# Kernel tuning notes

Hardware: AMD Instinct MI355X
Metric: run time of the kernel (lower is better)

Reference implementation:

```python
import jax, jax.numpy as jnp
import numpy as np

N_T = 8
N_R = 2
NOISE = 1e-12  # 10**(-120/10)
B = 65536


def setup_inputs() -> dict:
    key = jax.random.key(0)
    ks = jax.random.split(key, 7)
    return {
        "theta1": jax.random.normal(ks[0], (B, 264), dtype=jnp.float32),
        "G1r": jax.random.normal(ks[1], (B, N_R, 100), dtype=jnp.float32),
        "G1i": jax.random.normal(ks[2], (B, N_R, 100), dtype=jnp.float32),
        "G2r": jax.random.normal(ks[3], (B, N_R, 100), dtype=jnp.float32),
        "G2i": jax.random.normal(ks[4], (B, N_R, 100), dtype=jnp.float32),
        "Ur": jax.random.normal(ks[5], (B, 100, N_T), dtype=jnp.float32),
        "Ui": jax.random.normal(ks[6], (B, 100, N_T), dtype=jnp.float32),
    }


def _rate(phi, Fsig, Fintf):
    # phi: [B, N_r, N_t], Fsig/Fintf: [B, N_t, N_r]
    A = jnp.einsum("bnt,btr->bnr", phi, Fsig)    # signal term  [B, N_r, N_r]
    C = jnp.einsum("bnt,btr->bnr", phi, Fintf)   # interference [B, N_r, N_r]
    # Mu = C C^H + noise (elementwise scalar add, faithful to torch source)
    Mu = jnp.einsum("bnr,bmr->bnm", C, jnp.conj(C)) + NOISE
    inner = jnp.einsum("brn,bnm,bms->brs", jnp.conj(A).transpose(0, 2, 1) if False else jnp.conj(jnp.swapaxes(A, 1, 2)), jnp.linalg.inv(Mu), A)
    # note: torch does 1 + matrix (elementwise), not identity add
    return jnp.real(jnp.log(jnp.linalg.det(1.0 + inner)))  # [B]


def reference(theta1, G1r, G1i, G2r, G2i, Ur, Ui):
    M1N1 = N_T * N_R  # 16
    F1 = theta1[:, 200:200 + M1N1] + 1j * theta1[:, 200 + M1N1:200 + 2 * M1N1]
    F2 = theta1[:, 200 + 2 * M1N1:200 + 3 * M1N1] + 1j * theta1[:, 200 + 3 * M1N1:]
    # power normalization: F * sqrt(2 / (F^H F))
    F1 = F1 * jnp.sqrt(2.0 / jnp.sum(jnp.conj(F1) * F1, axis=1, keepdims=True))
    F2 = F2 * jnp.sqrt(2.0 / jnp.sum(jnp.conj(F2) * F2, axis=1, keepdims=True))
    F1m = F1.reshape(-1, N_T, N_R)
    F2m = F2.reshape(-1, N_T, N_R)

    theta = theta1[:, 0:100] + 1j * theta1[:, 100:200]  # [B, 100]
    G1 = G1r + 1j * G1i
    G2 = G2r + 1j * G2i
    U = Ur + 1j * Ui

    # phi = G @ diag(theta) @ U, vectorized over batch
    phi1 = jnp.einsum("bnk,bk,bkt->bnt", G1, theta, U)  # [B, N_r, N_t]
    phi2 = jnp.einsum("bnk,bk,bkt->bnt", G2, theta, U)

    R1 = _rate(phi1, F1m, F2m)
    R2 = _rate(phi2, F2m, F1m)
    R = jnp.maximum(-R1, -R2)
    return jnp.sum(R) / theta1.shape[0]
```

## Files before the change

### kernel.cpp

```cpp
#include <hip/hip_runtime.h>
#include <math.h>

#define NOISE 1e-12f
#define WSZ 1064
#define WSZ4 266

typedef float f32x2 __attribute__((ext_vector_type(2)));

__device__ __forceinline__ f32x2 mk2(float x, float y){ f32x2 r; r.x = x; r.y = y; return r; }

__device__ __forceinline__ f32x2 cmul_pk(f32x2 a, f32x2 b) {
    f32x2 w;
    asm("v_pk_mul_f32 %0, %1, %2 op_sel:[0,0] op_sel_hi:[0,1]\n\t"
        "v_pk_fma_f32 %0, %1, %2, %0 op_sel:[1,1,0] op_sel_hi:[1,0,1] neg_lo:[0,1,0]"
        : "=&v"(w) : "v"(a), "v"(b));
    return w;
}
__device__ __forceinline__ void cfma_pk(f32x2& p, f32x2 a, f32x2 w) {
    asm("v_pk_fma_f32 %0, %1, %2, %0 op_sel:[0,0,0] op_sel_hi:[0,1,1]\n\t"
        "v_pk_fma_f32 %0, %1, %2, %0 op_sel:[1,1,0] op_sel_hi:[1,0,1] neg_lo:[0,1,0]"
        : "+v"(p) : "v"(a), "v"(w));
}

__device__ __forceinline__ float2 cmul(float2 a, float2 b) {
    return make_float2(a.x*b.x - a.y*b.y, a.x*b.y + a.y*b.x);
}
__device__ __forceinline__ float2 cconjmul(float2 a, float2 b) {
    return make_float2(a.x*b.x + a.y*b.y, a.x*b.y - a.y*b.x);
}
__device__ __forceinline__ float2 cmulconj(float2 a, float2 b) {
    return make_float2(a.x*b.x + a.y*b.y, a.y*b.x - a.x*b.y);
}
__device__ __forceinline__ float2 cadd(float2 a, float2 b){ return make_float2(a.x+b.x, a.y+b.y); }
__device__ __forceinline__ float2 csub(float2 a, float2 b){ return make_float2(a.x-b.x, a.y-b.y); }
__device__ __forceinline__ float2 cscale(float s, float2 a){ return make_float2(s*a.x, s*a.y); }

typedef const void __attribute__((address_space(1)))* gas_t;
typedef void __attribute__((address_space(3)))* las_t;
__device__ __forceinline__ void gll4(const float* g, float* l) {
    __builtin_amdgcn_global_load_lds((gas_t)g, (las_t)l, 4, 0, 0);
}

__global__ __launch_bounds__(256) void rate_kernel(
    const float* __restrict__ t1,
    const float* __restrict__ G1r, const float* __restrict__ G1i,
    const float* __restrict__ G2r, const float* __restrict__ G2i,
    const float* __restrict__ Ur,  const float* __restrict__ Ui,
    float* __restrict__ partial)
{
    __shared__ float4 lds4[4 * WSZ4];
    __shared__ float2 ent[4][4][16];
    __shared__ float wsum[4];
    const int wave = threadIdx.x >> 6;
    const int lane = threadIdx.x & 63;
    const int t  = lane & 7;
    const int k0 = lane >> 3;
    const int e8 = k0;
    const int nn = (e8 >> 1) & 1;
    const int rr = e8 & 1;
    float* W = (float*)(lds4 + wave * WSZ4);
    const float4* F4 = (const float4*)W;

    const int half  = lane & 1;
    const int qh    = lane >> 1;

    #define STAGE(dst, bb) {                                                   \
        const float* tb_ = t1 + (long)(bb) * 264;                              \
        const float* ts  = tb_ + (half ? 100 : 0) + qh;                        \
        gll4(ts,       (dst));        gll4(ts + 32,  (dst) + 64);              \
        gll4(ts + 64,  (dst) + 128);                                           \
        if (lane < 8) gll4(ts + 96, (dst) + 192);                              \
        gll4(tb_ + 200 + lane, (dst) + 200);                                   \
        const float* g1 = (half ? G1i : G1r) + (long)(bb) * 200 + qh;          \
        const float* g2 = (half ? G2i : G2r) + (long)(bb) * 200 + qh;          \
        gll4(g1,        (dst)+264);   gll4(g1+32,  (dst)+328);                 \
        gll4(g1+64,     (dst)+392);   gll4(g1+96,  (dst)+456);                 \
        gll4(g1+128,    (dst)+520);   gll4(g1+160, (dst)+584);                 \
        if (lane < 16) gll4(g1+192, (dst)+648);                                \
        gll4(g2,        (dst)+664);   gll4(g2+32,  (dst)+728);                 \
        gll4(g2+64,     (dst)+792);   gll4(g2+96,  (dst)+856);                 \
        gll4(g2+128,    (dst)+920);   gll4(g2+160, (dst)+984);                 \
        if (lane < 16) gll4(g2+192, (dst)+1048);                               \
    }

    const long bbase = (long)blockIdx.x * 16 + (long)wave * 4;
    STAGE(W, bbase);

    const float* urb = Ur + bbase * 800;
    const float* uib = Ui + bbase * 800;
    const int uoff = 32 * k0 + t;
    #define LDU2(idx) mk2(urb[(idx)], uib[(idx)])

    f32x2 u0 = LDU2(uoff), u1 = LDU2(uoff+8), u2 = LDU2(uoff+16), u3 = LDU2(uoff+24);

    #define JGROUP_PK(f0, U0, U1, U2, U3) {                                   \
        float4 t01 = F4[(f0)],      t23 = F4[(f0)+1];                         \
        float4 a01 = F4[66+(f0)],   a23 = F4[67+(f0)];                        \
        float4 c01 = F4[116+(f0)],  c23 = F4[117+(f0)];                       \
        float4 d01 = F4[166+(f0)],  d23 = F4[167+(f0)];                       \
        float4 e01 = F4[216+(f0)],  e23 = F4[217+(f0)];                       \
        { f32x2 Wk = cmul_pk(mk2(t01.x,t01.y), U0);                           \
          cfma_pk(p10, mk2(a01.x,a01.y), Wk); cfma_pk(p11, mk2(c01.x,c01.y), Wk); \
          cfma_pk(p20, mk2(d01.x,d01.y), Wk); cfma_pk(p21, mk2(e01.x,e01.y), Wk); } \
        { f32x2 Wk = cmul_pk(mk2(t01.z,t01.w), U1);                           \
          cfma_pk(p10, mk2(a01.z,a01.w), Wk); cfma_pk(p11, mk2(c01.z,c01.w), Wk); \
          cfma_pk(p20, mk2(d01.z,d01.w), Wk); cfma_pk(p21, mk2(e01.z,e01.w), Wk); } \
        { f32x2 Wk = cmul_pk(mk2(t23.x,t23.y), U2);                           \
          cfma_pk(p10, mk2(a23.x,a23.y), Wk); cfma_pk(p11, mk2(c23.x,c23.y), Wk); \
          cfma_pk(p20, mk2(d23.x,d23.y), Wk); cfma_pk(p21, mk2(e23.x,e23.y), Wk); } \
        { f32x2 Wk = cmul_pk(mk2(t23.z,t23.w), U3);                           \
          cfma_pk(p10, mk2(a23.z,a23.w), Wk); cfma_pk(p11, mk2(c23.z,c23.w), Wk); \
          cfma_pk(p20, mk2(d23.z,d23.w), Wk); cfma_pk(p21, mk2(e23.z,e23.w), Wk); } }

    const int idxF = lane & 15;
    const int selF = (lane >> 4) & 1;
    const int jf   = t*2 + rr;

    for (int it = 0; it < 4; ++it) {
        asm volatile("s_waitcnt vmcnt(8)" ::: "memory");
        __builtin_amdgcn_sched_barrier(0);

        float fr = W[200 + selF*32 + idxF];
        float fi = W[216 + selF*32 + idxF];
        float2 f1 = make_float2(W[200 + jf], W[216 + jf]);
        float2 f2 = make_float2(W[232 + jf], W[248 + jf]);

        f32x2 p10 = mk2(0.f,0.f), p11 = mk2(0.f,0.f);
        f32x2 p20 = mk2(0.f,0.f), p21 = mk2(0.f,0.f);

        #pragma unroll 1
        for (int j = 0; j < 3; ++j) {
            f32x2 n0, n1, n2, n3;
            if (j < 2) {
                const int nb = uoff + 256 * (j + 1);
                n0 = LDU2(nb); n1 = LDU2(nb+8); n2 = LDU2(nb+16); n3 = LDU2(nb+24);
            } else {
                n0 = LDU2(768+t); n1 = LDU2(776+t); n2 = LDU2(784+t); n3 = LDU2(792+t);
            }
            JGROUP_PK(2*k0 + 16*j, u0, u1, u2, u3);
            u0 = n0; u1 = n1; u2 = n2; u3 = n3;
        }
        if (k0 == 0) {
            JGROUP_PK(48, u0, u1, u2, u3);
        }

        if (it < 3) {
            asm volatile("s_waitcnt lgkmcnt(0)" ::: "memory");
            __builtin_amdgcn_sched_barrier(0);
            STAGE(W, bbase + it + 1);
            __builtin_amdgcn_sched_barrier(0);
            urb += 800; uib += 800;
            u0 = LDU2(uoff); u1 = LDU2(uoff+8); u2 = LDU2(uoff+16); u3 = LDU2(uoff+24);
            __builtin_amdgcn_sched_barrier(0);
        }

        float p[8] = {p10.x, p10.y, p11.x, p11.y, p20.x, p20.y, p21.x, p21.y};
        #pragma unroll
        for (int q = 0; q < 8; ++q) {
            p[q] += __shfl_xor(p[q], 8);
            p[q] += __shfl_xor(p[q], 32);
        }
        float4 ph;
        {
            float k0r = nn ? p[2] : p[0], s0r = nn ? p[0] : p[2];
            float k0i = nn ? p[3] : p[1], s0i = nn ? p[1] : p[3];
            float k1r = nn ? p[6] : p[4], s1r = nn ? p[4] : p[6];
            float k1i = nn ? p[7] : p[5], s1i = nn ? p[5] : p[7];
            ph.x = k0r + __shfl_xor(s0r, 16);
            ph.y = k0i + __shfl_xor(s0i, 16);
            ph.z = k1r + __shfl_xor(s1r, 16);
            ph.w = k1i + __shfl_xor(s1i, 16);
        }

        float s1, s2;
        {
            float m = fr*fr + fi*fi;
            #pragma unroll
            for (int s = 1; s < 16; s <<= 1) m += __shfl_xor(m, s);
            float other = __shfl_xor(m, 16);
            float nrm1 = selF ? other : m;
            float nrm2 = selF ? m : other;
            s1 = sqrtf(2.0f / nrm1);
            s2 = sqrtf(2.0f / nrm2);
        }

        {
            float2 phi1n = make_float2(ph.x, ph.y);
            float2 phi2n = make_float2(ph.z, ph.w);
            bool lo = (e8 < 4);
            float2 E0 = cmul(phi1n, lo ? f1 : f2);
            float2 E1 = cmul(phi2n, lo ? f2 : f1);
            #pragma unroll
            for (int s = 1; s < 8; s <<= 1) {
                E0.x += __shfl_xor(E0.x, s); E0.y += __shfl_xor(E0.y, s);
                E1.x += __shfl_xor(E1.x, s); E1.y += __shfl_xor(E1.y, s);
            }
            if (t == 0) {
                ent[wave][it][e8]     = cscale(lo ? s1 : s2, E0);
                ent[wave][it][e8 + 8] = cscale(lo ? s2 : s1, E1);
            }
        }
    }
    #undef STAGE
    #undef LDU2
    #undef JGROUP_PK
    asm volatile("s_waitcnt lgkmcnt(0)" ::: "memory");
    __builtin_amdgcn_wave_barrier();

    float negR = 0.0f;
    if (lane < 8) {
        const float2* e = &ent[wave][lane >> 1][(lane & 1) * 8];
        float2 A00=e[0], A01=e[1], A10=e[2], A11=e[3];
        float2 C00=e[4], C01=e[5], C10=e[6], C11=e[7];
        float mu00 = C00.x*C00.x + C00.y*C00.y + C01.x*C01.x + C01.y*C01.y + NOISE;
        float mu11 = C10.x*C10.x + C10.y*C10.y + C11.x*C11.x + C11.y*C11.y + NOISE;
        float2 mu01 = cadd(cmulconj(C00, C10), cmulconj(C01, C11));
        mu01.x += NOISE;
        float det = mu00*mu11 - (mu01.x*mu01.x + mu01.y*mu01.y);
        float inv = 1.0f / det;
        float2 mu01c = make_float2(mu01.x, -mu01.y);
        float2 X00 = cscale(inv, csub(cscale(mu11, A00), cmul(mu01,  A10)));
        float2 X01 = cscale(inv, csub(cscale(mu11, A01), cmul(mu01,  A11)));
        float2 X10 = cscale(inv, csub(cscale(mu00, A10), cmul(mu01c, A00)));
        float2 X11 = cscale(inv, csub(cscale(mu00, A11), cmul(mu01c, A01)));
        float2 I00 = cadd(cconjmul(A00, X00), cconjmul(A10, X10));
        float2 I01 = cadd(cconjmul(A00, X01), cconjmul(A10, X11));
        float2 I10 = cadd(cconjmul(A01, X00), cconjmul(A11, X10));
        float2 I11 = cadd(cconjmul(A01, X01), cconjmul(A11, X11));
        I00.x += 1.0f; I01.x += 1.0f; I10.x += 1.0f; I11.x += 1.0f;
        float2 dT = csub(cmul(I00, I11), cmul(I01, I10));
        negR = -0.5f * logf(dT.x*dT.x + dT.y*dT.y);
    }
    float m = fmaxf(negR, __shfl_xor(negR, 1));
    m += __shfl_xor(m, 2);
    m += __shfl_xor(m, 4);
    if (lane == 0) wsum[wave] = m;

    __syncthreads();
    if (threadIdx.x == 0)
        partial[blockIdx.x] = (wsum[0] + wsum[1]) + (wsum[2] + wsum[3]);
}

__global__ __launch_bounds__(256) void reduce_kernel(
    const float* __restrict__ partial, int n, float invB, float* __restrict__ out)
{
    __shared__ float sd[256];
    float s = 0.0f;
    for (int i = threadIdx.x; i < n; i += 256) s += partial[i];
    sd[threadIdx.x] = s;
    __syncthreads();
    for (int o = 128; o > 0; o >>= 1) {
        if ((int)threadIdx.x < o) sd[threadIdx.x] += sd[threadIdx.x + o];
        __syncthreads();
    }
    if (threadIdx.x == 0) out[0] = sd[0] * invB;
}

extern "C" void kernel_launch(void* const* d_in, const int* in_sizes, int n_in,
                              void* d_out, int out_size, void* d_ws, size_t ws_size,
                              hipStream_t stream) {
    const float* t1  = (const float*)d_in[0];
    const float* G1r = (const float*)d_in[1];
    const float* G1i = (const float*)d_in[2];
    const float* G2r = (const float*)d_in[3];
    const float* G2i = (const float*)d_in[4];
    const float* Ur  = (const float*)d_in[5];
    const float* Ui  = (const float*)d_in[6];

    const int B = in_sizes[0] / 264;
    const int nblocks = B / 16;
    float* partial = (float*)d_ws;

    rate_kernel<<<nblocks, 256, 0, stream>>>(t1, G1r, G1i, G2r, G2i, Ur, Ui, partial);
    reduce_kernel<<<1, 256, 0, stream>>>(partial, nblocks, 1.0f / (float)B, (float*)d_out);
}
```

Before: 138.3 us.

## Remap lanes to 16 k-rows by 4 t-pairs with float2 U loads

Changes the per-lane work mapping in the phi = G·diag(theta)·U contraction. Each lane now handles 2 adjacent t columns and strides k by 32, so U is loaded as float2 and each theta/G pair from LDS is reused across two columns. The cross-lane reduction tree and the final F-projection are rebuilt to match the new layout. This is meant to cut LDS reads and global load instructions per FMA, at the cost of more accumulator registers and a reworked shuffle sequence.

Result: faster. 135.0 us (-2.4%).

```diff
diff --git a/kernel.cpp b/kernel.cpp
--- a/kernel.cpp
+++ b/kernel.cpp
@@ -53,13 +53,9 @@
     __shared__ float wsum[4];
     const int wave = threadIdx.x >> 6;
     const int lane = threadIdx.x & 63;
-    const int t  = lane & 7;
-    const int k0 = lane >> 3;
-    const int e8 = k0;
-    const int nn = (e8 >> 1) & 1;
-    const int rr = e8 & 1;
+    const int t2 = lane & 3;
+    const int k0 = lane >> 2;
     float* W = (float*)(lds4 + wave * WSZ4);
-    const float4* F4 = (const float4*)W;
 
     const int half  = lane & 1;
     const int qh    = lane >> 1;
@@ -88,61 +84,58 @@
 
     const float* urb = Ur + bbase * 800;
     const float* uib = Ui + bbase * 800;
-    const int uoff = 32 * k0 + t;
-    #define LDU2(idx) mk2(urb[(idx)], uib[(idx)])
-
-    f32x2 u0 = LDU2(uoff), u1 = LDU2(uoff+8), u2 = LDU2(uoff+16), u3 = LDU2(uoff+24);
-
-    #define JGROUP_PK(f0, U0, U1, U2, U3) {                                   \
-        float4 t01 = F4[(f0)],      t23 = F4[(f0)+1];                         \
-        float4 a01 = F4[66+(f0)],   a23 = F4[67+(f0)];                        \
-        float4 c01 = F4[116+(f0)],  c23 = F4[117+(f0)];                       \
-        float4 d01 = F4[166+(f0)],  d23 = F4[167+(f0)];                       \
-        float4 e01 = F4[216+(f0)],  e23 = F4[217+(f0)];                       \
-        { f32x2 Wk = cmul_pk(mk2(t01.x,t01.y), U0);                           \
-          cfma_pk(p10, mk2(a01.x,a01.y), Wk); cfma_pk(p11, mk2(c01.x,c01.y), Wk); \
-          cfma_pk(p20, mk2(d01.x,d01.y), Wk); cfma_pk(p21, mk2(e01.x,e01.y), Wk); } \
-        { f32x2 Wk = cmul_pk(mk2(t01.z,t01.w), U1);                           \
-          cfma_pk(p10, mk2(a01.z,a01.w), Wk); cfma_pk(p11, mk2(c01.z,c01.w), Wk); \
-          cfma_pk(p20, mk2(d01.z,d01.w), Wk); cfma_pk(p21, mk2(e01.z,e01.w), Wk); } \
-        { f32x2 Wk = cmul_pk(mk2(t23.x,t23.y), U2);                           \
-          cfma_pk(p10, mk2(a23.x,a23.y), Wk); cfma_pk(p11, mk2(c23.x,c23.y), Wk); \
-          cfma_pk(p20, mk2(d23.x,d23.y), Wk); cfma_pk(p21, mk2(e23.x,e23.y), Wk); } \
-        { f32x2 Wk = cmul_pk(mk2(t23.z,t23.w), U3);                           \
-          cfma_pk(p10, mk2(a23.z,a23.w), Wk); cfma_pk(p11, mk2(c23.z,c23.w), Wk); \
-          cfma_pk(p20, mk2(d23.z,d23.w), Wk); cfma_pk(p21, mk2(e23.z,e23.w), Wk); } }
+    const int ubase = 8 * k0 + 2 * t2;
+    const int utail = 8 * (96 + (k0 < 4 ? k0 : 3)) + 2 * t2;
+    #define LD2(p, idx) (*(const float2*)((p) + (idx)))
+
+    float2 g0r = LD2(urb, ubase),       g0i = LD2(uib, ubase);
+    float2 g1r = LD2(urb, ubase+128),   g1i = LD2(uib, ubase+128);
+    float2 g2r = LD2(urb, ubase+256),   g2i = LD2(uib, ubase+256);
+    float2 g3r = LD2(urb, ubase+384),   g3i = LD2(uib, ubase+384);
+
+    #define JBODY(j, gr, gi) {                                        \
+        const int kk = 2*k0 + 32*(j);                                 \
+        f32x2 th = *(const f32x2*)(W + kk);                           \
+        f32x2 ga = *(const f32x2*)(W + 264 + kk);                     \
+        f32x2 gc = *(const f32x2*)(W + 464 + kk);                     \
+        f32x2 gd = *(const f32x2*)(W + 664 + kk);                     \
+        f32x2 ge = *(const f32x2*)(W + 864 + kk);                     \
+        f32x2 w0 = cmul_pk(th, mk2((gr).x, (gi).x));                  \
+        f32x2 w1 = cmul_pk(th, mk2((gr).y, (gi).y));                  \
+        cfma_pk(p10a, ga, w0);  cfma_pk(p10b, ga, w1);                \
+        cfma_pk(p11a, gc, w0);  cfma_pk(p11b, gc, w1);                \
+        cfma_pk(p20a, gd, w0);  cfma_pk(p20b, gd, w1);                \
+        cfma_pk(p21a, ge, w0);  cfma_pk(p21b, ge, w1); }
 
     const int idxF = lane & 15;
     const int selF = (lane >> 4) & 1;
-    const int jf   = t*2 + rr;
-
+    const bool useF1 = (k0 < 4) || (k0 >= 12);
+    const int fb = useF1 ? 200 : 232;
+    const int i0 = 4*t2 + (k0 & 1);
+
+    #pragma unroll 1
     for (int it = 0; it < 4; ++it) {
         asm volatile("s_waitcnt vmcnt(8)" ::: "memory");
         __builtin_amdgcn_sched_barrier(0);
 
         float fr = W[200 + selF*32 + idxF];
         float fi = W[216 + selF*32 + idxF];
-        float2 f1 = make_float2(W[200 + jf], W[216 + jf]);
-        float2 f2 = make_float2(W[232 + jf], W[248 + jf]);
-
-        f32x2 p10 = mk2(0.f,0.f), p11 = mk2(0.f,0.f);
-        f32x2 p20 = mk2(0.f,0.f), p21 = mk2(0.f,0.f);
-
-        #pragma unroll 1
-        for (int j = 0; j < 3; ++j) {
-            f32x2 n0, n1, n2, n3;
-            if (j < 2) {
-                const int nb = uoff + 256 * (j + 1);
-                n0 = LDU2(nb); n1 = LDU2(nb+8); n2 = LDU2(nb+16); n3 = LDU2(nb+24);
-            } else {
-                n0 = LDU2(768+t); n1 = LDU2(776+t); n2 = LDU2(784+t); n3 = LDU2(792+t);
-            }
-            JGROUP_PK(2*k0 + 16*j, u0, u1, u2, u3);
-            u0 = n0; u1 = n1; u2 = n2; u3 = n3;
-        }
-        if (k0 == 0) {
-            JGROUP_PK(48, u0, u1, u2, u3);
-        }
+        float2 fv0 = make_float2(W[fb + i0],     W[fb + 16 + i0]);
+        float2 fv1 = make_float2(W[fb + i0 + 2], W[fb + 18 + i0]);
+
+        f32x2 p10a=mk2(0,0), p10b=mk2(0,0), p11a=mk2(0,0), p11b=mk2(0,0);
+        f32x2 p20a=mk2(0,0), p20b=mk2(0,0), p21a=mk2(0,0), p21b=mk2(0,0);
+
+        float2 g4r = LD2(urb, ubase+512), g4i = LD2(uib, ubase+512);
+        JBODY(0, g0r, g0i);
+        float2 g5r = LD2(urb, ubase+640), g5i = LD2(uib, ubase+640);
+        JBODY(1, g1r, g1i);
+        float2 g6r = LD2(urb, utail),     g6i = LD2(uib, utail);
+        JBODY(2, g2r, g2i);
+        JBODY(3, g3r, g3i);
+        JBODY(4, g4r, g4i);
+        JBODY(5, g5r, g5i);
+        if (k0 < 4) JBODY(6, g6r, g6i);
 
         if (it < 3) {
             asm volatile("s_waitcnt lgkmcnt(0)" ::: "memory");
@@ -150,60 +143,60 @@
             STAGE(W, bbase + it + 1);
             __builtin_amdgcn_sched_barrier(0);
             urb += 800; uib += 800;
-            u0 = LDU2(uoff); u1 = LDU2(uoff+8); u2 = LDU2(uoff+16); u3 = LDU2(uoff+24);
+            g0r = LD2(urb, ubase);     g0i = LD2(uib, ubase);
+            g1r = LD2(urb, ubase+128); g1i = LD2(uib, ubase+128);
+            g2r = LD2(urb, ubase+256); g2i = LD2(uib, ubase+256);
+            g3r = LD2(urb, ubase+384); g3i = LD2(uib, ubase+384);
             __builtin_amdgcn_sched_barrier(0);
         }
 
-        float p[8] = {p10.x, p10.y, p11.x, p11.y, p20.x, p20.y, p21.x, p21.y};
-        #pragma unroll
-        for (int q = 0; q < 8; ++q) {
-            p[q] += __shfl_xor(p[q], 8);
-            p[q] += __shfl_xor(p[q], 32);
+        float q[16] = {p10a.x,p10a.y,p10b.x,p10b.y,
+                       p11a.x,p11a.y,p11b.x,p11b.y,
+                       p20a.x,p20a.y,p20b.x,p20b.y,
+                       p21a.x,p21a.y,p21b.x,p21b.y};
+        #pragma unroll
+        for (int i = 0; i < 16; ++i) q[i] += __shfl_xor(q[i], 4);
+        const int nsel = (lane >> 3) & 1;
+        float r8[8];
+        #pragma unroll
+        for (int i = 0; i < 4; ++i) {
+            float ka = nsel ? q[4+i]  : q[i];
+            float sa = nsel ? q[i]    : q[4+i];
+            r8[i]   = ka + __shfl_xor(sa, 8);
+            float kb = nsel ? q[12+i] : q[8+i];
+            float sb = nsel ? q[8+i]  : q[12+i];
+            r8[4+i] = kb + __shfl_xor(sb, 8);
         }
-        float4 ph;
-        {
-            float k0r = nn ? p[2] : p[0], s0r = nn ? p[0] : p[2];
-            float k0i = nn ? p[3] : p[1], s0i = nn ? p[1] : p[3];
-            float k1r = nn ? p[6] : p[4], s1r = nn ? p[4] : p[6];
-            float k1i = nn ? p[7] : p[5], s1i = nn ? p[5] : p[7];
-            ph.x = k0r + __shfl_xor(s0r, 16);
-            ph.y = k0i + __shfl_xor(s0i, 16);
-            ph.z = k1r + __shfl_xor(s1r, 16);
-            ph.w = k1i + __shfl_xor(s1i, 16);
+        #pragma unroll
+        for (int i = 0; i < 8; ++i) r8[i] += __shfl_xor(r8[i], 16);
+        const int msel = (lane >> 5) & 1;
+        float ph[4];
+        #pragma unroll
+        for (int i = 0; i < 4; ++i) {
+            float kp = msel ? r8[4+i] : r8[i];
+            float sp = msel ? r8[i]   : r8[4+i];
+            ph[i] = kp + __shfl_xor(sp, 32);
         }
 
-        float s1, s2;
-        {
-            float m = fr*fr + fi*fi;
-            #pragma unroll
-            for (int s = 1; s < 16; s <<= 1) m += __shfl_xor(m, s);
-            float other = __shfl_xor(m, 16);
-            float nrm1 = selF ? other : m;
-            float nrm2 = selF ? m : other;
-            s1 = sqrtf(2.0f / nrm1);
-            s2 = sqrtf(2.0f / nrm2);
-        }
-
-        {
-            float2 phi1n = make_float2(ph.x, ph.y);
-            float2 phi2n = make_float2(ph.z, ph.w);
-            bool lo = (e8 < 4);
-            float2 E0 = cmul(phi1n, lo ? f1 : f2);
-            float2 E1 = cmul(phi2n, lo ? f2 : f1);
-            #pragma unroll
-            for (int s = 1; s < 8; s <<= 1) {
-                E0.x += __shfl_xor(E0.x, s); E0.y += __shfl_xor(E0.y, s);
-                E1.x += __shfl_xor(E1.x, s); E1.y += __shfl_xor(E1.y, s);
-            }
-            if (t == 0) {
-                ent[wave][it][e8]     = cscale(lo ? s1 : s2, E0);
-                ent[wave][it][e8 + 8] = cscale(lo ? s2 : s1, E1);
-            }
-        }
+        float m = fr*fr + fi*fi;
+        #pragma unroll
+        for (int s = 1; s < 16; s <<= 1) m += __shfl_xor(m, s);
+        float other = __shfl_xor(m, 16);
+        float nrm1 = selF ? other : m;
+        float nrm2 = selF ? m : other;
+        float sc1 = sqrtf(2.0f / nrm1);
+        float sc2 = sqrtf(2.0f / nrm2);
+        float sE = useF1 ? sc1 : sc2;
+
+        float2 E = cadd(cmul(make_float2(ph[0], ph[1]), fv0),
+                        cmul(make_float2(ph[2], ph[3]), fv1));
+        E.x += __shfl_xor(E.x, 1); E.y += __shfl_xor(E.y, 1);
+        E.x += __shfl_xor(E.x, 2); E.y += __shfl_xor(E.y, 2);
+        if (t2 == 0) ent[wave][it][k0] = cscale(sE, E);
     }
     #undef STAGE
-    #undef LDU2
-    #undef JGROUP_PK
+    #undef LD2
+    #undef JBODY
     asm volatile("s_waitcnt lgkmcnt(0)" ::: "memory");
     __builtin_amdgcn_wave_barrier();
 
```
